# Kernel optimization log

Measured on AMD Instinct MI355X. Metric: run time of the kernel, lower is better.

## Reference

```python
import jax, jax.numpy as jnp
import numpy as np

TAU = 1.0
PAD_IDX = 0
EOS_IDX = 3
NEG = -10000000.0

B, T, H, E, V, BN = 256, 256, 1024, 512, 32000, 512


def setup_inputs() -> dict:
    key = jax.random.key(0)
    ks = jax.random.split(key, 30)
    s = lambda *sh: 0.02
    inp = {}
    inp['input_ids'] = jax.random.randint(ks[0], (B,), 0, V)
    inp['prediction'] = jax.random.normal(ks[1], (B, V), jnp.float32)
    inp['context'] = jax.random.normal(ks[2], (B, T, 2 * H), jnp.float32)
    inp['h0'] = jax.random.normal(ks[3], (2, B, H), jnp.float32)
    inp['mask'] = jax.random.randint(ks[4], (B, 8), 0, V)
    # parameters
    inp['embedding'] = jax.random.normal(ks[5], (V, E), jnp.float32) * 0.02
    inp['ge1_w'] = jax.random.normal(ks[6], (E, E), jnp.float32) * 0.02
    inp['ge1_b'] = jnp.zeros((E,), jnp.float32)
    inp['ge2_w'] = jax.random.normal(ks[7], (E, E), jnp.float32) * 0.02
    inp['ge2_b'] = jnp.zeros((E,), jnp.float32)
    inp['att_we'] = jax.random.normal(ks[8], (2 * H, H), jnp.float32) * 0.02
    inp['att_wd'] = jax.random.normal(ks[9], (H, H), jnp.float32) * 0.02
    inp['att_v'] = jax.random.normal(ks[10], (H,), jnp.float32) * 0.02
    in0 = 2 * H + E
    inp['wih0'] = jax.random.normal(ks[11], (3 * H, in0), jnp.float32) * 0.02
    inp['whh0'] = jax.random.normal(ks[12], (3 * H, H), jnp.float32) * 0.02
    inp['bih0'] = jnp.zeros((3 * H,), jnp.float32)
    inp['bhh0'] = jnp.zeros((3 * H,), jnp.float32)
    inp['wih1'] = jax.random.normal(ks[13], (3 * H, H), jnp.float32) * 0.02
    inp['whh1'] = jax.random.normal(ks[14], (3 * H, H), jnp.float32) * 0.02
    inp['bih1'] = jnp.zeros((3 * H,), jnp.float32)
    inp['bhh1'] = jnp.zeros((3 * H,), jnp.float32)
    inp['bn0_w'] = jax.random.normal(ks[15], (3 * H + E, BN), jnp.float32) * 0.02
    inp['bn0_b'] = jnp.zeros((BN,), jnp.float32)
    inp['bn1_w'] = jax.random.normal(ks[16], (BN, V), jnp.float32) * 0.02
    inp['bn1_b'] = jnp.zeros((V,), jnp.float32)
    return inp


def _gru_cell(x, h, wih, whh, bih, bhh):
    gi = x @ wih.T + bih  # [B, 3H]
    gh = h @ whh.T + bhh
    gi_r, gi_z, gi_n = jnp.split(gi, 3, axis=1)
    gh_r, gh_z, gh_n = jnp.split(gh, 3, axis=1)
    r = jax.nn.sigmoid(gi_r + gh_r)
    z = jax.nn.sigmoid(gi_z + gh_z)
    n = jnp.tanh(gi_n + r * gh_n)
    return (1.0 - z) * n + z * h


def _forward(input_ids, prediction, context, h0, mask, embedding,
             ge1_w, ge1_b, ge2_w, ge2_b, att_we, att_wd, att_v,
             wih0, whh0, bih0, bhh0, wih1, whh1, bih1, bhh1,
             bn0_w, bn0_b, bn1_w, bn1_b):
    embs = embedding[input_ids]  # [B, E]
    # global embedding gate
    probs = jax.nn.softmax(prediction / TAU, axis=1)  # [B, V]
    emb_avg = probs @ embedding  # [B, E]
    Hg = jax.nn.sigmoid(embs @ ge1_w + ge1_b + emb_avg @ ge2_w + ge2_b)
    embs = Hg * embs + (1.0 - Hg) * emb_avg
    # bahdanau attention with query = top-layer hidden
    q = h0[-1]  # [B, H]
    scores = jnp.tanh(context @ att_we + (q @ att_wd)[:, None, :]) @ att_v  # [B, T]
    attn = jax.nn.softmax(scores, axis=1)
    c_t = jnp.einsum('bt,btd->bd', attn, context)  # [B, 2H]
    rnn_in = jnp.concatenate([embs, c_t], axis=1)  # [B, E+2H]
    h1_0 = _gru_cell(rnn_in, h0[0], wih0, whh0, bih0, bhh0)
    h1_1 = _gru_cell(h1_0, h0[1], wih1, whh1, bih1, bhh1)
    output = h1_1
    h1 = jnp.stack([h1_0, h1_1])
    b0 = jnp.tanh(jnp.concatenate([output, c_t, embs], axis=1) @ bn0_w + bn0_b)
    pred = b0 @ bn1_w + bn1_b  # [B, V]
    # masked scatter: forbid already-generated tokens, but keep PAD/EOS columns
    pad_col = pred[:, PAD_IDX]
    eos_col = pred[:, EOS_IDX]
    rows = jnp.arange(pred.shape[0])
    pred = pred.at[rows[:, None], mask].set(NEG)
    pred = pred.at[:, PAD_IDX].set(pad_col)
    pred = pred.at[:, EOS_IDX].set(eos_col)
    return pred, h1, attn


def reference(input_ids, prediction, context, h0, mask, embedding,
              ge1_w, ge1_b, ge2_w, ge2_b, att_we, att_wd, att_v,
              wih0, whh0, bih0, bhh0, wih1, whh1, bih1, bhh1,
              bn0_w, bn0_b, bn1_w, bn1_b):
    return _forward(input_ids, prediction, context, h0, mask, embedding,
                    ge1_w, ge1_b, ge2_w, ge2_b, att_we, att_wd, att_v,
                    wih0, whh0, bih0, bhh0, wih1, whh1, bih1, bhh1,
                    bn0_w, bn0_b, bn1_w, bn1_b)
```

## Files before the change

### kernel.cpp

```cpp
#include <hip/hip_runtime.h>
#include <hip/hip_bf16.h>


typedef unsigned short u16;
typedef unsigned int u32;
typedef float f32x4 __attribute__((ext_vector_type(4)));
typedef u32 u32x4 __attribute__((ext_vector_type(4)));
typedef __bf16 bf16x8 __attribute__((ext_vector_type(8)));
typedef short s16x8 __attribute__((ext_vector_type(8)));

__device__ __forceinline__ u16 f2bf(float x) {
  u32 u = __float_as_uint(x);
  u += 0x7fffu + ((u >> 16) & 1u);
  return (u16)(u >> 16);
}
__device__ __forceinline__ u32 pack2(float a, float b) {
  return (u32)f2bf(a) | ((u32)f2bf(b) << 16);
}
__device__ __forceinline__ u32 cvt2(float a, float b) {
  union { __bf16 h[2]; u32 w; } u;
  u.h[0] = (__bf16)a; u.h[1] = (__bf16)b;
  return u.w;
}
__device__ __forceinline__ float bf2f(u16 v) {
  return __uint_as_float((u32)v << 16);
}
__device__ __forceinline__ f32x4 mfma_bf16(s16x8 a, s16x8 b, f32x4 c) {
  union { s16x8 s; bf16x8 b; } ua, ub;
  ua.s = a; ub.s = b;
  return __builtin_amdgcn_mfma_f32_16x16x32_bf16(ua.b, ub.b, c, 0, 0, 0);
}
__device__ __forceinline__ void gll16(const void* g, void* l) {
  __builtin_amdgcn_global_load_lds((__attribute__((address_space(1))) void*)g,
                                   (__attribute__((address_space(3))) void*)l,
                                   16, 0, 0);
}
__device__ __forceinline__ float sigf(float x) { return 1.0f / (1.0f + __expf(-x)); }

__global__ __launch_bounds__(256) void k_cvt8(const float* __restrict__ s,
                                              u16* __restrict__ d)
{
  size_t i = ((size_t)blockIdx.x * 256 + threadIdx.x) * 8;
  const size_t stride = (size_t)gridDim.x * 2048;
  for (; i < 134217728ull; i += stride) {
    float4 a = *(const float4*)(s + i);
    float4 b = *(const float4*)(s + i + 4);
    u32x4 w = {cvt2(a.x, a.y), cvt2(a.z, a.w), cvt2(b.x, b.y), cvt2(b.z, b.w)};
    *(u32x4*)(d + i) = w;
  }
}

__global__ __launch_bounds__(512, 4) void k_scores_bf(
    const u16* __restrict__ A, const u16* __restrict__ weT,
    const float* __restrict__ qd, const float* __restrict__ att_v,
    float* __restrict__ scores)
{
  __shared__ u16 As[2][4096];
  __shared__ u16 Bs[2][8192];

  const int tid = threadIdx.x;
  const int lane = tid & 63, wid = tid >> 6;
  const int l15 = lane & 15, lg = lane >> 4;
  const int wm = wid >> 2, wn = wid & 3;
  const int n0 = blockIdx.x * 256;
  const int m0 = blockIdx.y * 128;
  const int b = blockIdx.y >> 1;

  const int sslot = ((lane & 3) ^ ((lane >> 3) & 3)) * 8;
  const size_t asrc = (size_t)(m0 + wid * 16 + (lane >> 2)) * 2048 + sslot;
  size_t bsrc[2];
#pragma unroll
  for (int i = 0; i < 2; ++i)
    bsrc[i] = (size_t)(n0 + (wid * 2 + i) * 16 + (lane >> 2)) * 2048 + sslot;

  const int rslot = (lg ^ ((l15 >> 1) & 3)) * 8;
  int aoff[4], boff[4];
#pragma unroll
  for (int mf = 0; mf < 4; ++mf) aoff[mf] = (wm * 64 + mf * 16 + l15) * 32 + rslot;
#pragma unroll
  for (int nf = 0; nf < 4; ++nf) boff[nf] = (wn * 64 + nf * 16 + l15) * 32 + rslot;

  f32x4 acc[4][4];
#pragma unroll
  for (int mf = 0; mf < 4; ++mf)
#pragma unroll
    for (int nf = 0; nf < 4; ++nf) acc[mf][nf] = (f32x4){0.f, 0.f, 0.f, 0.f};

  {
    gll16(A + asrc, &As[0][wid * 512]);
#pragma unroll
    for (int i = 0; i < 2; ++i)
      gll16(weT + bsrc[i], &Bs[0][(wid * 2 + i) * 512]);
  }
  __syncthreads();

  for (int kt = 0; kt < 64; ++kt) {
    const int cur = kt & 1, nxt = cur ^ 1;
    if (kt < 63) {
      gll16(A + asrc + (size_t)(kt + 1) * 32, &As[nxt][wid * 512]);
#pragma unroll
      for (int i = 0; i < 2; ++i)
        gll16(weT + bsrc[i] + (size_t)(kt + 1) * 32, &Bs[nxt][(wid * 2 + i) * 512]);
    }
    s16x8 af[4], bf[4];
#pragma unroll
    for (int mf = 0; mf < 4; ++mf) af[mf] = *(const s16x8*)(&As[cur][0] + aoff[mf]);
#pragma unroll
    for (int nf = 0; nf < 4; ++nf) bf[nf] = *(const s16x8*)(&Bs[cur][0] + boff[nf]);
    __builtin_amdgcn_s_setprio(1);
#pragma unroll
    for (int nf = 0; nf < 4; ++nf)
#pragma unroll
      for (int mf = 0; mf < 4; ++mf)
        acc[mf][nf] = mfma_bf16(af[mf], bf[nf], acc[mf][nf]);
    __builtin_amdgcn_s_setprio(0);
    __syncthreads();
  }

  float rp[4][4] = {{0.f, 0.f, 0.f, 0.f}, {0.f, 0.f, 0.f, 0.f},
                    {0.f, 0.f, 0.f, 0.f}, {0.f, 0.f, 0.f, 0.f}};
#pragma unroll
  for (int nf = 0; nf < 4; ++nf) {
    int col = n0 + wn * 64 + nf * 16 + l15;
    float qv = qd[(size_t)b * 1024 + col];
    float vv = att_v[col];
#pragma unroll
    for (int mf = 0; mf < 4; ++mf)
#pragma unroll
      for (int e = 0; e < 4; ++e)
        rp[mf][e] += tanhf(acc[mf][nf][e] + qv) * vv;
  }
#pragma unroll
  for (int d = 1; d < 16; d <<= 1)
#pragma unroll
    for (int mf = 0; mf < 4; ++mf)
#pragma unroll
      for (int e = 0; e < 4; ++e)
        rp[mf][e] += __shfl_xor(rp[mf][e], d);
  if (l15 == 0) {
#pragma unroll
    for (int mf = 0; mf < 4; ++mf)
#pragma unroll
      for (int e = 0; e < 4; ++e)
        atomicAdd(&scores[(size_t)m0 + wm * 64 + mf * 16 + lg * 4 + e], rp[mf][e]);
  }
}

__global__ __launch_bounds__(256, 3) void k_scores(
    const float* __restrict__ ctx, const u16* __restrict__ weT,
    const float* __restrict__ qd, const float* __restrict__ att_v,
    float* __restrict__ scores)
{
  __shared__ u16 As[2][4096];
  __shared__ u16 Bs[2][4096];

  const int tid = threadIdx.x;
  const int lane = tid & 63, wid = tid >> 6;
  const int l15 = lane & 15, lg = lane >> 4;
  const int wm = wid >> 1, wn = wid & 1;
  const int n0 = blockIdx.x * 128;
  const int m0 = blockIdx.y * 128;
  const int b = blockIdx.y >> 1;

  const int r0 = tid >> 3, c4 = tid & 7;
  const float* actx = ctx + (size_t)(m0 + r0) * 2048 + c4 * 4;
  const int awoff = r0 * 32 + c4 * 4;

  size_t bsrc[2];
#pragma unroll
  for (int i = 0; i < 2; ++i)
    bsrc[i] = (size_t)(n0 + (wid * 2 + i) * 16 + (lane >> 2)) * 2048 + (size_t)(lane & 3) * 8;

  int aoff[4], boff[4];
#pragma unroll
  for (int mf = 0; mf < 4; ++mf) aoff[mf] = (wm * 64 + mf * 16 + l15) * 32 + lg * 8;
#pragma unroll
  for (int nf = 0; nf < 4; ++nf) boff[nf] = (wn * 64 + nf * 16 + l15) * 32 + lg * 8;

  f32x4 acc[4][4];
#pragma unroll
  for (int mf = 0; mf < 4; ++mf)
#pragma unroll
    for (int nf = 0; nf < 4; ++nf) acc[mf][nf] = (f32x4){0.f, 0.f, 0.f, 0.f};

  {
#pragma unroll
    for (int i = 0; i < 2; ++i)
      gll16(weT + bsrc[i], &Bs[0][(wid * 2 + i) * 512]);
#pragma unroll
    for (int j = 0; j < 4; ++j) {
      float4 av = *(const float4*)(actx + (size_t)(j * 32) * 2048);
      u32* w = (u32*)&As[0][awoff + j * 1024];
      w[0] = cvt2(av.x, av.y); w[1] = cvt2(av.z, av.w);
    }
  }
  __syncthreads();

  for (int kt = 0; kt < 64; ++kt) {
    const int cur = kt & 1, nxt = cur ^ 1;
    const bool pf = (kt < 63);
    float4 av[4];
    if (pf) {
#pragma unroll
      for (int i = 0; i < 2; ++i)
        gll16(weT + bsrc[i] + (size_t)(kt + 1) * 32, &Bs[nxt][(wid * 2 + i) * 512]);
#pragma unroll
      for (int j = 0; j < 4; ++j)
        av[j] = *(const float4*)(actx + (size_t)(j * 32) * 2048 + (kt + 1) * 32);
    }
    s16x8 af[4], bf[4];
#pragma unroll
    for (int mf = 0; mf < 4; ++mf) af[mf] = *(const s16x8*)(&As[cur][0] + aoff[mf]);
#pragma unroll
    for (int nf = 0; nf < 4; ++nf) bf[nf] = *(const s16x8*)(&Bs[cur][0] + boff[nf]);
#pragma unroll
    for (int nf = 0; nf < 4; ++nf)
#pragma unroll
      for (int mf = 0; mf < 4; ++mf)
        acc[mf][nf] = mfma_bf16(af[mf], bf[nf], acc[mf][nf]);
    if (pf) {
#pragma unroll
      for (int j = 0; j < 4; ++j) {
        u32* w = (u32*)&As[nxt][awoff + j * 1024];
        w[0] = cvt2(av[j].x, av[j].y); w[1] = cvt2(av[j].z, av[j].w);
      }
    }
    __syncthreads();
  }

  float rp[4][4] = {{0.f, 0.f, 0.f, 0.f}, {0.f, 0.f, 0.f, 0.f},
                    {0.f, 0.f, 0.f, 0.f}, {0.f, 0.f, 0.f, 0.f}};
#pragma unroll
  for (int nf = 0; nf < 4; ++nf) {
    int col = n0 + wn * 64 + nf * 16 + l15;
    float qv = qd[(size_t)b * 1024 + col];
    float vv = att_v[col];
#pragma unroll
    for (int mf = 0; mf < 4; ++mf)
#pragma unroll
      for (int e = 0; e < 4; ++e)
        rp[mf][e] += tanhf(acc[mf][nf][e] + qv) * vv;
  }
#pragma unroll
  for (int d = 1; d < 16; d <<= 1)
#pragma unroll
    for (int mf = 0; mf < 4; ++mf)
#pragma unroll
      for (int e = 0; e < 4; ++e)
        rp[mf][e] += __shfl_xor(rp[mf][e], d);
  if (l15 == 0) {
#pragma unroll
    for (int mf = 0; mf < 4; ++mf)
#pragma unroll
      for (int e = 0; e < 4; ++e)
        atomicAdd(&scores[(size_t)m0 + wm * 64 + mf * 16 + lg * 4 + e], rp[mf][e]);
  }
}

template <int MODE>
__global__ __launch_bounds__(256, 2) void k_gemm(
    const u16* __restrict__ A, const float* __restrict__ W,
    float* __restrict__ C, const float* __restrict__ bias,
    int N, int K, int ksteps_per, int tot_ksteps, int atomic_mode)
{
  __shared__ u16 As[2][8192];
  __shared__ u16 Bs[2][2048];
  const int tid = threadIdx.x, lane = tid & 63, wid = tid >> 6;
  const int l15 = lane & 15, lg = lane >> 4;
  const int m0 = blockIdx.x * 256;
  const int n0 = blockIdx.y * 64;
  const int kc0 = blockIdx.z * ksteps_per;
  int kcn = tot_ksteps - kc0;
  if (kcn > ksteps_per) kcn = ksteps_per;

  size_t asrc[4];
#pragma unroll
  for (int j = 0; j < 4; ++j)
    asrc[j] = (size_t)(m0 + wid * 64 + j * 16 + (lane >> 2)) * K + (size_t)(lane & 3) * 8;
  int aoff[4], boff[4];
#pragma unroll
  for (int mf = 0; mf < 4; ++mf) aoff[mf] = (wid * 64 + mf * 16 + l15) * 32 + lg * 8;
#pragma unroll
  for (int nf = 0; nf < 4; ++nf) boff[nf] = (nf * 16 + l15) * 32 + lg * 8;

  const int b_row = tid >> 2, b_c8 = tid & 3;
  const int b_kk = tid >> 3, b_c4 = tid & 7;

  f32x4 acc[4][4];
#pragma unroll
  for (int mf = 0; mf < 4; ++mf)
#pragma unroll
    for (int nf = 0; nf < 4; ++nf) acc[mf][nf] = (f32x4){0.f, 0.f, 0.f, 0.f};

  {
#pragma unroll
    for (int j = 0; j < 4; ++j)
      gll16(A + asrc[j] + (size_t)kc0 * 32, &As[0][wid * 2048 + j * 512]);
    if (MODE == 0) {
      const float* p = W + (size_t)(n0 + b_row) * K + (size_t)kc0 * 32 + b_c8 * 8;
      float4 v0 = *(const float4*)p, v1 = *(const float4*)(p + 4);
      u32* w = (u32*)&Bs[0][b_row * 32 + b_c8 * 8];
      w[0] = pack2(v0.x, v0.y); w[1] = pack2(v0.z, v0.w);
      w[2] = pack2(v1.x, v1.y); w[3] = pack2(v1.z, v1.w);
    } else {
      const float* p = W + (size_t)(kc0 * 32 + b_kk) * N + n0 + b_c4 * 4;
      float4 v0 = *(const float4*)p;
      float4 v1 = *(const float4*)(p + 32);
      int r0 = b_c4 * 4, r1 = 32 + b_c4 * 4;
      Bs[0][(r0 + 0) * 32 + b_kk] = f2bf(v0.x);
      Bs[0][(r0 + 1) * 32 + b_kk] = f2bf(v0.y);
      Bs[0][(r0 + 2) * 32 + b_kk] = f2bf(v0.z);
      Bs[0][(r0 + 3) * 32 + b_kk] = f2bf(v0.w);
      Bs[0][(r1 + 0) * 32 + b_kk] = f2bf(v1.x);
      Bs[0][(r1 + 1) * 32 + b_kk] = f2bf(v1.y);
      Bs[0][(r1 + 2) * 32 + b_kk] = f2bf(v1.z);
      Bs[0][(r1 + 3) * 32 + b_kk] = f2bf(v1.w);
    }
  }
  __syncthreads();

  for (int s = 0; s < kcn; ++s) {
    const int cur = s & 1, nxt = cur ^ 1;
    const bool pf = (s + 1 < kcn);
    const int ktn = kc0 + s + 1;
    float4 v0, v1;
    if (pf) {
#pragma unroll
      for (int j = 0; j < 4; ++j)
        gll16(A + asrc[j] + (size_t)ktn * 32, &As[nxt][wid * 2048 + j * 512]);
      if (MODE == 0) {
        const float* p = W + (size_t)(n0 + b_row) * K + (size_t)ktn * 32 + b_c8 * 8;
        v0 = *(const float4*)p; v1 = *(const float4*)(p + 4);
      } else {
        const float* p = W + (size_t)(ktn * 32 + b_kk) * N + n0 + b_c4 * 4;
        v0 = *(const float4*)p;
        v1 = *(const float4*)(p + 32);
      }
    }
    s16x8 af[4], bf[4];
#pragma unroll
    for (int mf = 0; mf < 4; ++mf) af[mf] = *(const s16x8*)(&As[cur][0] + aoff[mf]);
#pragma unroll
    for (int nf = 0; nf < 4; ++nf) bf[nf] = *(const s16x8*)(&Bs[cur][0] + boff[nf]);
#pragma unroll
    for (int nf = 0; nf < 4; ++nf)
#pragma unroll
      for (int mf = 0; mf < 4; ++mf)
        acc[mf][nf] = mfma_bf16(af[mf], bf[nf], acc[mf][nf]);
    if (pf) {
      if (MODE == 0) {
        u32* w = (u32*)&Bs[nxt][b_row * 32 + b_c8 * 8];
        w[0] = pack2(v0.x, v0.y); w[1] = pack2(v0.z, v0.w);
        w[2] = pack2(v1.x, v1.y); w[3] = pack2(v1.z, v1.w);
      } else {
        int r0 = b_c4 * 4, r1 = 32 + b_c4 * 4;
        Bs[nxt][(r0 + 0) * 32 + b_kk] = f2bf(v0.x);
        Bs[nxt][(r0 + 1) * 32 + b_kk] = f2bf(v0.y);
        Bs[nxt][(r0 + 2) * 32 + b_kk] = f2bf(v0.z);
        Bs[nxt][(r0 + 3) * 32 + b_kk] = f2bf(v0.w);
        Bs[nxt][(r1 + 0) * 32 + b_kk] = f2bf(v1.x);
        Bs[nxt][(r1 + 1) * 32 + b_kk] = f2bf(v1.y);
        Bs[nxt][(r1 + 2) * 32 + b_kk] = f2bf(v1.z);
        Bs[nxt][(r1 + 3) * 32 + b_kk] = f2bf(v1.w);
      }
    }
    __syncthreads();
  }

  const size_t Ns = (size_t)N;
#pragma unroll
  for (int mf = 0; mf < 4; ++mf)
#pragma unroll
    for (int nf = 0; nf < 4; ++nf) {
      int col = n0 + nf * 16 + l15;
#pragma unroll
      for (int e = 0; e < 4; ++e) {
        int row = m0 + wid * 64 + mf * 16 + lg * 4 + e;
        float v = acc[mf][nf][e];
        if (atomic_mode) atomicAdd(&C[row * Ns + col], v);
        else C[row * Ns + col] = v + (bias ? bias[col] : 0.0f);
      }
    }
}

__global__ __launch_bounds__(256) void k_twe(const float* __restrict__ we, u16* __restrict__ weT)
{
  __shared__ float t[32][33];
  const int n0 = blockIdx.x * 32, k0 = blockIdx.y * 32;
  const int tid = threadIdx.x;
#pragma unroll
  for (int p = 0; p < 4; ++p) {
    int e = tid + p * 256, r = e >> 5, c = e & 31;
    t[r][c] = we[(size_t)(k0 + r) * 1024 + n0 + c];
  }
  __syncthreads();
#pragma unroll
  for (int p = 0; p < 4; ++p) {
    int e = tid + p * 256, n = e >> 5, k = e & 31;
    weT[(size_t)(n0 + n) * 2048 + k0 + k] = f2bf(t[k][n]);
  }
}

__global__ void k_cast(const float* __restrict__ s, u16* __restrict__ d, int n)
{
  int i = blockIdx.x * 256 + threadIdx.x;
  if (i < n) d[i] = f2bf(s[i]);
}

__global__ void k_gather(const int* __restrict__ ids, const float* __restrict__ emb,
                         float* __restrict__ e0, u16* __restrict__ e0b)
{
  int b = blockIdx.x, tid = threadIdx.x;
  int id = ids[b];
  for (int i = tid; i < 512; i += 256) {
    float v = emb[(size_t)id * 512 + i];
    e0[(size_t)b * 512 + i] = v;
    e0b[(size_t)b * 512 + i] = f2bf(v);
  }
}

__global__ __launch_bounds__(256) void k_softmax_pred(const float* __restrict__ pred,
                                                      u16* __restrict__ probs)
{
  __shared__ float sm[4];
  const int row = blockIdx.x, tid = threadIdx.x;
  const float* x = pred + (size_t)row * 32000;
  float mx = -1e30f;
  for (int i = tid; i < 32000; i += 256) mx = fmaxf(mx, x[i]);
#pragma unroll
  for (int d = 1; d < 64; d <<= 1) mx = fmaxf(mx, __shfl_xor(mx, d));
  if ((tid & 63) == 0) sm[tid >> 6] = mx;
  __syncthreads();
  mx = fmaxf(fmaxf(sm[0], sm[1]), fmaxf(sm[2], sm[3]));
  float s = 0.f;
  for (int i = tid; i < 32000; i += 256) s += __expf(x[i] - mx);
#pragma unroll
  for (int d = 1; d < 64; d <<= 1) s += __shfl_xor(s, d);
  __syncthreads();
  if ((tid & 63) == 0) sm[tid >> 6] = s;
  __syncthreads();
  s = sm[0] + sm[1] + sm[2] + sm[3];
  float inv = 1.0f / s;
  for (int i = tid; i < 32000; i += 256)
    probs[(size_t)row * 32000 + i] = f2bf(__expf(x[i] - mx) * inv);
}

__global__ __launch_bounds__(256) void k_softmax_sc(const float* __restrict__ sc,
                                                    float* __restrict__ attn)
{
  __shared__ float sm[4];
  const int row = blockIdx.x, tid = threadIdx.x;
  float x = sc[(size_t)row * 256 + tid];
  float mx = x;
#pragma unroll
  for (int d = 1; d < 64; d <<= 1) mx = fmaxf(mx, __shfl_xor(mx, d));
  if ((tid & 63) == 0) sm[tid >> 6] = mx;
  __syncthreads();
  mx = fmaxf(fmaxf(sm[0], sm[1]), fmaxf(sm[2], sm[3]));
  float e = __expf(x - mx);
  float s = e;
#pragma unroll
  for (int d = 1; d < 64; d <<= 1) s += __shfl_xor(s, d);
  __syncthreads();
  if ((tid & 63) == 0) sm[tid >> 6] = s;
  __syncthreads();
  s = sm[0] + sm[1] + sm[2] + sm[3];
  attn[(size_t)row * 256 + tid] = e / s;
}

__global__ __launch_bounds__(256) void k_ct_bf(const u16* __restrict__ ctxb,
                                               const float* __restrict__ attn,
                                               float* __restrict__ c_t)
{
  const int b = blockIdx.y;
  const int d0 = blockIdx.x * 512 + threadIdx.x * 2;
  const u16* cp = ctxb + (size_t)b * 524288 + d0;
  const float* ar = attn + (size_t)b * 256;
  float a0 = 0.f, a1 = 0.f;
#pragma unroll 8
  for (int t = 0; t < 256; ++t) {
    float a = ar[t];
    ushort2 v = *(const ushort2*)(cp + (size_t)t * 2048);
    a0 += a * bf2f(v.x); a1 += a * bf2f(v.y);
  }
  float2* o = (float2*)(c_t + (size_t)b * 2048 + d0);
  *o = (float2){a0, a1};
}

__global__ __launch_bounds__(256) void k_ct(const float* __restrict__ ctx,
                                            const float* __restrict__ attn,
                                            float* __restrict__ c_t)
{
  const int b = blockIdx.y;
  const int d0 = blockIdx.x * 512 + threadIdx.x * 2;
  const float2* cp = (const float2*)(ctx + (size_t)b * 524288 + d0);
  const float* ar = attn + (size_t)b * 256;
  float ax = 0.f, ay = 0.f;
#pragma unroll 4
  for (int t = 0; t < 256; ++t) {
    float a = ar[t];
    float2 v = cp[(size_t)t * 1024];
    ax += a * v.x; ay += a * v.y;
  }
  c_t[(size_t)b * 2048 + d0] = ax;
  c_t[(size_t)b * 2048 + d0 + 1] = ay;
}

__global__ void k_gate(const float* __restrict__ gepre, const float* __restrict__ b1,
                       const float* __restrict__ b2, const float* __restrict__ e0,
                       const float* __restrict__ ea, float* __restrict__ embs)
{
  int i = blockIdx.x * 256 + threadIdx.x;
  int nn = i & 511;
  float hg = sigf(gepre[i] + b1[nn] + b2[nn]);
  embs[i] = hg * e0[i] + (1.0f - hg) * ea[i];
}

__global__ void k_cat_rnn(const float* __restrict__ embs, const float* __restrict__ ct,
                          u16* __restrict__ out)
{
  int i = blockIdx.x * 256 + threadIdx.x;
  int m = i / 2560, c = i - m * 2560;
  float v = (c < 512) ? embs[(size_t)m * 512 + c] : ct[(size_t)m * 2048 + (c - 512)];
  out[i] = f2bf(v);
}

__global__ void k_gru(const float* __restrict__ gi, const float* __restrict__ gh,
                      const float* __restrict__ bih, const float* __restrict__ bhh,
                      const float* __restrict__ hprev, float* __restrict__ hout,
                      u16* __restrict__ hout_bf)
{
  int i = blockIdx.x * 256 + threadIdx.x;
  int m = i >> 10, h = i & 1023;
  const float* gim = gi + (size_t)m * 3072;
  const float* ghm = gh + (size_t)m * 3072;
  float r = sigf(gim[h] + bih[h] + ghm[h] + bhh[h]);
  float z = sigf(gim[1024 + h] + bih[1024 + h] + ghm[1024 + h] + bhh[1024 + h]);
  float n = tanhf(gim[2048 + h] + bih[2048 + h] + r * (ghm[2048 + h] + bhh[2048 + h]));
  float hv = (1.0f - z) * n + z * hprev[i];
  hout[i] = hv;
  if (hout_bf) hout_bf[i] = f2bf(hv);
}

__global__ void k_cat_bn0(const float* __restrict__ h11, const float* __restrict__ ct,
                          const float* __restrict__ embs, u16* __restrict__ out)
{
  int i = blockIdx.x * 256 + threadIdx.x;
  int m = i / 3584, c = i - m * 3584;
  float v;
  if (c < 1024) v = h11[(size_t)m * 1024 + c];
  else if (c < 3072) v = ct[(size_t)m * 2048 + (c - 1024)];
  else v = embs[(size_t)m * 512 + (c - 3072)];
  out[i] = f2bf(v);
}

__global__ void k_bn0(const float* __restrict__ pre, const float* __restrict__ bias,
                      u16* __restrict__ b0b)
{
  int i = blockIdx.x * 256 + threadIdx.x;
  int nn = i & 511;
  b0b[i] = f2bf(tanhf(pre[i] + bias[nn]));
}

__global__ void k_mask(const int* __restrict__ mask, float* __restrict__ pred)
{
  int t = blockIdx.x * 256 + threadIdx.x;
  if (t >= 2048) return;
  int b = t >> 3;
  int col = mask[t];
  if (col != 0 && col != 3) pred[(size_t)b * 32000 + col] = -10000000.0f;
}

extern "C" void kernel_launch(void* const* d_in, const int* in_sizes, int n_in,
                              void* d_out, int out_size, void* d_ws, size_t ws_size,
                              hipStream_t stream)
{
  const int*   input_ids = (const int*)d_in[0];
  const float* prediction= (const float*)d_in[1];
  const float* context   = (const float*)d_in[2];
  const float* h0        = (const float*)d_in[3];
  const int*   maskp     = (const int*)d_in[4];
  const float* embedding = (const float*)d_in[5];
  const float* ge1_w = (const float*)d_in[6];
  const float* ge1_b = (const float*)d_in[7];
  const float* ge2_w = (const float*)d_in[8];
  const float* ge2_b = (const float*)d_in[9];
  const float* att_we = (const float*)d_in[10];
  const float* att_wd = (const float*)d_in[11];
  const float* att_v  = (const float*)d_in[12];
  const float* wih0 = (const float*)d_in[13];
  const float* whh0 = (const float*)d_in[14];
  const float* bih0 = (const float*)d_in[15];
  const float* bhh0 = (const float*)d_in[16];
  const float* wih1 = (const float*)d_in[17];
  const float* whh1 = (const float*)d_in[18];
  const float* bih1 = (const float*)d_in[19];
  const float* bhh1 = (const float*)d_in[20];
  const float* bn0_w = (const float*)d_in[21];
  const float* bn0_b = (const float*)d_in[22];
  const float* bn1_w = (const float*)d_in[23];
  const float* bn1_b = (const float*)d_in[24];

  float* out = (float*)d_out;
  float* out_pred = out;
  float* out_h1_0 = out + 8192000;
  float* out_h1_1 = out + 8454144;
  float* out_attn = out + 8716288;

  char* ws = (char*)d_ws;
  float* qd      = (float*)(ws + 0);
  float* emb_avg = (float*)(ws + 1048576);
  float* gepre   = (float*)(ws + 1572864);
  float* gi0     = (float*)(ws + 2097152);
  float* gh0     = (float*)(ws + 5242880);
  float* gi1     = (float*)(ws + 8388608);
  float* gh1     = (float*)(ws + 11534336);
  float* bn0pre  = (float*)(ws + 14680064);
  float* scores  = (float*)(ws + 15204352);
  const size_t MS_BYTES = 15466496;
  float* c_t     = (float*)(ws + 15466496);
  float* embs0   = (float*)(ws + 17563648);
  float* embs    = (float*)(ws + 18087936);
  u16* weT       = (u16*)(ws + 18612224);
  u16* h0_bf     = (u16*)(ws + 22806528);
  u16* embs0_bf  = (u16*)(ws + 23855104);
  u16* probs_bf  = (u16*)(ws + 24117248);
  u16* embavg_bf = (u16*)(ws + 40501248);
  u16* rnnin_bf  = (u16*)(ws + 40763392);
  u16* h1_0_bf   = (u16*)(ws + 42074112);
  u16* bn0in_bf  = (u16*)(ws + 42598400);
  u16* b0_bf     = (u16*)(ws + 44433408);
  u16* ctx_bf    = (u16*)(ws + 44695552);
  const bool big = ws_size >= 44695552ull + 268435456ull;

  (void)in_sizes; (void)n_in; (void)out_size;

  hipMemsetAsync(ws, 0, MS_BYTES, stream);

  if (big) k_cvt8<<<8192, 256, 0, stream>>>(context, ctx_bf);
  k_twe<<<dim3(32, 64), 256, 0, stream>>>(att_we, weT);
  k_cast<<<2048, 256, 0, stream>>>(h0, h0_bf, 524288);
  k_gather<<<256, 256, 0, stream>>>(input_ids, embedding, embs0, embs0_bf);
  k_softmax_pred<<<256, 256, 0, stream>>>(prediction, probs_bf);

  k_gemm<1><<<dim3(1, 16, 8), 256, 0, stream>>>(h0_bf + 262144, att_wd, qd, nullptr,
                                                1024, 1024, 4, 32, 1);
  if (big)
    k_scores_bf<<<dim3(4, 512), 512, 0, stream>>>(ctx_bf, weT, qd, att_v, scores);
  else
    k_scores<<<dim3(8, 512), 256, 0, stream>>>(context, weT, qd, att_v, scores);

  k_gemm<1><<<dim3(1, 8, 50), 256, 0, stream>>>(probs_bf, embedding, emb_avg, nullptr,
                                                512, 32000, 20, 1000, 1);
  k_cast<<<512, 256, 0, stream>>>(emb_avg, embavg_bf, 131072);
  k_gemm<1><<<dim3(1, 8, 4), 256, 0, stream>>>(embs0_bf, ge1_w, gepre, nullptr,
                                               512, 512, 4, 16, 1);
  k_gemm<1><<<dim3(1, 8, 4), 256, 0, stream>>>(embavg_bf, ge2_w, gepre, nullptr,
                                               512, 512, 4, 16, 1);
  k_gate<<<512, 256, 0, stream>>>(gepre, ge1_b, ge2_b, embs0, emb_avg, embs);

  k_softmax_sc<<<256, 256, 0, stream>>>(scores, out_attn);
  if (big)
    k_ct_bf<<<dim3(4, 256), 256, 0, stream>>>(ctx_bf, out_attn, c_t);
  else
    k_ct<<<dim3(4, 256), 256, 0, stream>>>(context, out_attn, c_t);

  k_cat_rnn<<<2560, 256, 0, stream>>>(embs, c_t, rnnin_bf);
  k_gemm<0><<<dim3(1, 48, 5), 256, 0, stream>>>(rnnin_bf, wih0, gi0, nullptr,
                                                3072, 2560, 16, 80, 1);
  k_gemm<0><<<dim3(1, 48, 4), 256, 0, stream>>>(h0_bf, whh0, gh0, nullptr,
                                                3072, 1024, 8, 32, 1);
  k_gru<<<1024, 256, 0, stream>>>(gi0, gh0, bih0, bhh0, h0, out_h1_0, h1_0_bf);
  k_gemm<0><<<dim3(1, 48, 4), 256, 0, stream>>>(h1_0_bf, wih1, gi1, nullptr,
                                                3072, 1024, 8, 32, 1);
  k_gemm<0><<<dim3(1, 48, 4), 256, 0, stream>>>(h0_bf + 262144, whh1, gh1, nullptr,
                                                3072, 1024, 8, 32, 1);
  k_gru<<<1024, 256, 0, stream>>>(gi1, gh1, bih1, bhh1, h0 + 262144, out_h1_1, nullptr);

  k_cat_bn0<<<3584, 256, 0, stream>>>(out_h1_1, c_t, embs, bn0in_bf);
  k_gemm<1><<<dim3(1, 8, 16), 256, 0, stream>>>(bn0in_bf, bn0_w, bn0pre, nullptr,
                                                512, 3584, 7, 112, 1);
  k_bn0<<<512, 256, 0, stream>>>(bn0pre, bn0_b, b0_bf);
  k_gemm<1><<<dim3(1, 500, 1), 256, 0, stream>>>(b0_bf, bn1_w, out_pred, bn1_b,
                                                 32000, 512, 16, 16, 0);
  k_mask<<<8, 256, 0, stream>>>(maskp, out_pred);
}
```

Before: 885.2 us.

## Triple-buffer scores GEMM, remap tiles per XCD, fuse small prep and softmax kernels

The attention-scores GEMM moves from double to triple buffering, waiting on vmcnt instead of a full syncthreads, and its 1D grid is remapped so M tiles are spread across XCDs. The weight transpose, h0 cast and embedding gather are merged into one prep kernel. Attention softmax is fused into the context-vector kernel, and the gate is fused with the RNN-input concat. The prediction softmax now uses 1024 threads, an online max/sum in one pass and an LDS-cached bf16 copy of the row. Together these aim to cut launch count, global re-reads and per-step sync stalls, at the cost of more LDS use and softmax inputs rounded to bf16 before exp.

```diff
diff --git a/kernel.cpp b/kernel.cpp
--- a/kernel.cpp
+++ b/kernel.cpp
@@ -55,16 +55,21 @@
     const float* __restrict__ qd, const float* __restrict__ att_v,
     float* __restrict__ scores)
 {
-  __shared__ u16 As[2][4096];
-  __shared__ u16 Bs[2][8192];
+  __shared__ u16 As[3][4096];
+  __shared__ u16 Bs[3][8192];
 
   const int tid = threadIdx.x;
   const int lane = tid & 63, wid = tid >> 6;
   const int l15 = lane & 15, lg = lane >> 4;
   const int wm = wid >> 2, wn = wid & 3;
-  const int n0 = blockIdx.x * 256;
-  const int m0 = blockIdx.y * 128;
-  const int b = blockIdx.y >> 1;
+
+  const int f = blockIdx.x;
+  const int xcd = f & 7, slot = f >> 3;
+  const int ntile = slot & 3;
+  const int mtile = (slot >> 2) * 8 + xcd;
+  const int n0 = ntile * 256;
+  const int m0 = mtile * 128;
+  const int b = mtile >> 1;
 
   const int sslot = ((lane & 3) ^ ((lane >> 3) & 3)) * 8;
   const size_t asrc = (size_t)(m0 + wid * 16 + (lane >> 2)) * 2048 + sslot;
@@ -86,27 +91,40 @@
 #pragma unroll
     for (int nf = 0; nf < 4; ++nf) acc[mf][nf] = (f32x4){0.f, 0.f, 0.f, 0.f};
 
+  u16* As0 = &As[0][0];
+  u16* Bs0 = &Bs[0][0];
+
   {
-    gll16(A + asrc, &As[0][wid * 512]);
+    gll16(A + asrc, As0 + wid * 512);
 #pragma unroll
     for (int i = 0; i < 2; ++i)
-      gll16(weT + bsrc[i], &Bs[0][(wid * 2 + i) * 512]);
-  }
-  __syncthreads();
-
+      gll16(weT + bsrc[i], Bs0 + (wid * 2 + i) * 512);
+    gll16(A + asrc + 32, As0 + 4096 + wid * 512);
+#pragma unroll
+    for (int i = 0; i < 2; ++i)
+      gll16(weT + bsrc[i] + 32, Bs0 + 8192 + (wid * 2 + i) * 512);
+  }
+
+  int cur = 0, stg = 2;
   for (int kt = 0; kt < 64; ++kt) {
-    const int cur = kt & 1, nxt = cur ^ 1;
-    if (kt < 63) {
-      gll16(A + asrc + (size_t)(kt + 1) * 32, &As[nxt][wid * 512]);
+    if (kt < 63) asm volatile("s_waitcnt vmcnt(3)" ::: "memory");
+    else         asm volatile("s_waitcnt vmcnt(0)" ::: "memory");
+    __builtin_amdgcn_s_barrier();
+    __builtin_amdgcn_sched_barrier(0);
+    if (kt + 2 < 64) {
+      gll16(A + asrc + (size_t)(kt + 2) * 32, As0 + stg * 4096 + wid * 512);
 #pragma unroll
       for (int i = 0; i < 2; ++i)
-        gll16(weT + bsrc[i] + (size_t)(kt + 1) * 32, &Bs[nxt][(wid * 2 + i) * 512]);
+        gll16(weT + bsrc[i] + (size_t)(kt + 2) * 32,
+              Bs0 + stg * 8192 + (wid * 2 + i) * 512);
     }
     s16x8 af[4], bf[4];
 #pragma unroll
-    for (int mf = 0; mf < 4; ++mf) af[mf] = *(const s16x8*)(&As[cur][0] + aoff[mf]);
-#pragma unroll
-    for (int nf = 0; nf < 4; ++nf) bf[nf] = *(const s16x8*)(&Bs[cur][0] + boff[nf]);
+    for (int mf = 0; mf < 4; ++mf)
+      af[mf] = *(const s16x8*)(As0 + cur * 4096 + aoff[mf]);
+#pragma unroll
+    for (int nf = 0; nf < 4; ++nf)
+      bf[nf] = *(const s16x8*)(Bs0 + cur * 8192 + boff[nf]);
     __builtin_amdgcn_s_setprio(1);
 #pragma unroll
     for (int nf = 0; nf < 4; ++nf)
@@ -114,7 +132,8 @@
       for (int mf = 0; mf < 4; ++mf)
         acc[mf][nf] = mfma_bf16(af[mf], bf[nf], acc[mf][nf]);
     __builtin_amdgcn_s_setprio(0);
-    __syncthreads();
+    cur = (cur == 2) ? 0 : cur + 1;
+    stg = (stg == 2) ? 0 : stg + 1;
   }
 
   float rp[4][4] = {{0.f, 0.f, 0.f, 0.f}, {0.f, 0.f, 0.f, 0.f},
@@ -383,21 +402,38 @@
     }
 }
 
-__global__ __launch_bounds__(256) void k_twe(const float* __restrict__ we, u16* __restrict__ weT)
+__global__ __launch_bounds__(256) void k_prep(
+    const float* __restrict__ we, u16* __restrict__ weT,
+    const float* __restrict__ h0, u16* __restrict__ h0_bf,
+    const int* __restrict__ ids, const float* __restrict__ emb,
+    float* __restrict__ e0, u16* __restrict__ e0b)
 {
   __shared__ float t[32][33];
-  const int n0 = blockIdx.x * 32, k0 = blockIdx.y * 32;
-  const int tid = threadIdx.x;
-#pragma unroll
-  for (int p = 0; p < 4; ++p) {
-    int e = tid + p * 256, r = e >> 5, c = e & 31;
-    t[r][c] = we[(size_t)(k0 + r) * 1024 + n0 + c];
-  }
-  __syncthreads();
-#pragma unroll
-  for (int p = 0; p < 4; ++p) {
-    int e = tid + p * 256, n = e >> 5, k = e & 31;
-    weT[(size_t)(n0 + n) * 2048 + k0 + k] = f2bf(t[k][n]);
+  const int bid = blockIdx.x, tid = threadIdx.x;
+  if (bid < 2048) {
+    const int n0 = (bid & 31) * 32, k0 = (bid >> 5) * 32;
+#pragma unroll
+    for (int p = 0; p < 4; ++p) {
+      int e = tid + p * 256, r = e >> 5, c = e & 31;
+      t[r][c] = we[(size_t)(k0 + r) * 1024 + n0 + c];
+    }
+    __syncthreads();
+#pragma unroll
+    for (int p = 0; p < 4; ++p) {
+      int e = tid + p * 256, n = e >> 5, k = e & 31;
+      weT[(size_t)(n0 + n) * 2048 + k0 + k] = f2bf(t[k][n]);
+    }
+  } else if (bid < 4096) {
+    int i = (bid - 2048) * 256 + tid;
+    h0_bf[i] = f2bf(h0[i]);
+  } else {
+    int b = bid - 4096;
+    int id = ids[b];
+    for (int i = tid; i < 512; i += 256) {
+      float v = emb[(size_t)id * 512 + i];
+      e0[(size_t)b * 512 + i] = v;
+      e0b[(size_t)b * 512 + i] = f2bf(v);
+    }
   }
 }
 
@@ -407,42 +443,39 @@
   if (i < n) d[i] = f2bf(s[i]);
 }
 
-__global__ void k_gather(const int* __restrict__ ids, const float* __restrict__ emb,
-                         float* __restrict__ e0, u16* __restrict__ e0b)
-{
-  int b = blockIdx.x, tid = threadIdx.x;
-  int id = ids[b];
-  for (int i = tid; i < 512; i += 256) {
-    float v = emb[(size_t)id * 512 + i];
-    e0[(size_t)b * 512 + i] = v;
-    e0b[(size_t)b * 512 + i] = f2bf(v);
-  }
-}
-
-__global__ __launch_bounds__(256) void k_softmax_pred(const float* __restrict__ pred,
-                                                      u16* __restrict__ probs)
-{
-  __shared__ float sm[4];
+__global__ __launch_bounds__(1024) void k_softmax_pred(const float* __restrict__ pred,
+                                                       u16* __restrict__ probs)
+{
+  __shared__ u16 xrow[32000];
+  __shared__ float smM[16], smS[16];
   const int row = blockIdx.x, tid = threadIdx.x;
   const float* x = pred + (size_t)row * 32000;
-  float mx = -1e30f;
-  for (int i = tid; i < 32000; i += 256) mx = fmaxf(mx, x[i]);
-#pragma unroll
-  for (int d = 1; d < 64; d <<= 1) mx = fmaxf(mx, __shfl_xor(mx, d));
-  if ((tid & 63) == 0) sm[tid >> 6] = mx;
-  __syncthreads();
-  mx = fmaxf(fmaxf(sm[0], sm[1]), fmaxf(sm[2], sm[3]));
-  float s = 0.f;
-  for (int i = tid; i < 32000; i += 256) s += __expf(x[i] - mx);
-#pragma unroll
-  for (int d = 1; d < 64; d <<= 1) s += __shfl_xor(s, d);
-  __syncthreads();
-  if ((tid & 63) == 0) sm[tid >> 6] = s;
-  __syncthreads();
-  s = sm[0] + sm[1] + sm[2] + sm[3];
-  float inv = 1.0f / s;
-  for (int i = tid; i < 32000; i += 256)
-    probs[(size_t)row * 32000 + i] = f2bf(__expf(x[i] - mx) * inv);
+  float m = -3.0e38f, s = 0.f;
+  for (int i = tid; i < 32000; i += 1024) {
+    u16 bv = f2bf(x[i]);
+    xrow[i] = bv;
+    float vr = bf2f(bv);
+    if (vr > m) { s = s * __expf(m - vr) + 1.0f; m = vr; }
+    else s += __expf(vr - m);
+  }
+#pragma unroll
+  for (int d = 1; d < 64; d <<= 1) {
+    float mo = __shfl_xor(m, d), so = __shfl_xor(s, d);
+    float M = fmaxf(m, mo);
+    s = s * __expf(m - M) + so * __expf(mo - M);
+    m = M;
+  }
+  if ((tid & 63) == 0) { smM[tid >> 6] = m; smS[tid >> 6] = s; }
+  __syncthreads();
+  float M = -3.0e38f;
+#pragma unroll
+  for (int w = 0; w < 16; ++w) M = fmaxf(M, smM[w]);
+  float S = 0.f;
+#pragma unroll
+  for (int w = 0; w < 16; ++w) S += smS[w] * __expf(smM[w] - M);
+  float inv = 1.0f / S;
+  for (int i = tid; i < 32000; i += 1024)
+    probs[(size_t)row * 32000 + i] = f2bf(__expf(bf2f(xrow[i]) - M) * inv);
 }
 
 __global__ __launch_bounds__(256) void k_softmax_sc(const float* __restrict__ sc,
@@ -468,20 +501,41 @@
   attn[(size_t)row * 256 + tid] = e / s;
 }
 
-__global__ __launch_bounds__(256) void k_ct_bf(const u16* __restrict__ ctxb,
-                                               const float* __restrict__ attn,
-                                               float* __restrict__ c_t)
-{
-  const int b = blockIdx.y;
-  const int d0 = blockIdx.x * 512 + threadIdx.x * 2;
+__global__ __launch_bounds__(256) void k_attn_ct(
+    const float* __restrict__ sc, const u16* __restrict__ ctxb,
+    float* __restrict__ attn, float* __restrict__ c_t)
+{
+  __shared__ float sm[4];
+  __shared__ float att[256];
+  const int b = blockIdx.y, tid = threadIdx.x;
+  float x = sc[(size_t)b * 256 + tid];
+  float mx = x;
+#pragma unroll
+  for (int d = 1; d < 64; d <<= 1) mx = fmaxf(mx, __shfl_xor(mx, d));
+  if ((tid & 63) == 0) sm[tid >> 6] = mx;
+  __syncthreads();
+  mx = fmaxf(fmaxf(sm[0], sm[1]), fmaxf(sm[2], sm[3]));
+  float e = __expf(x - mx);
+  float s = e;
+#pragma unroll
+  for (int d = 1; d < 64; d <<= 1) s += __shfl_xor(s, d);
+  __syncthreads();
+  if ((tid & 63) == 0) sm[tid >> 6] = s;
+  __syncthreads();
+  s = sm[0] + sm[1] + sm[2] + sm[3];
+  float a = e / s;
+  att[tid] = a;
+  if (blockIdx.x == 0) attn[(size_t)b * 256 + tid] = a;
+  __syncthreads();
+
+  const int d0 = blockIdx.x * 512 + tid * 2;
   const u16* cp = ctxb + (size_t)b * 524288 + d0;
-  const float* ar = attn + (size_t)b * 256;
   float a0 = 0.f, a1 = 0.f;
 #pragma unroll 8
   for (int t = 0; t < 256; ++t) {
-    float a = ar[t];
+    float av = att[t];
     ushort2 v = *(const ushort2*)(cp + (size_t)t * 2048);
-    a0 += a * bf2f(v.x); a1 += a * bf2f(v.y);
+    a0 += av * bf2f(v.x); a1 += av * bf2f(v.y);
   }
   float2* o = (float2*)(c_t + (size_t)b * 2048 + d0);
   *o = (float2){a0, a1};
@@ -506,22 +560,22 @@
   c_t[(size_t)b * 2048 + d0 + 1] = ay;
 }
 
-__global__ void k_gate(const float* __restrict__ gepre, const float* __restrict__ b1,
-                       const float* __restrict__ b2, const float* __restrict__ e0,
-                       const float* __restrict__ ea, float* __restrict__ embs)
-{
-  int i = blockIdx.x * 256 + threadIdx.x;
-  int nn = i & 511;
-  float hg = sigf(gepre[i] + b1[nn] + b2[nn]);
-  embs[i] = hg * e0[i] + (1.0f - hg) * ea[i];
-}
-
-__global__ void k_cat_rnn(const float* __restrict__ embs, const float* __restrict__ ct,
-                          u16* __restrict__ out)
+__global__ void k_gate_cat(const float* __restrict__ gepre, const float* __restrict__ b1,
+                           const float* __restrict__ b2, const float* __restrict__ e0,
+                           const float* __restrict__ ea, float* __restrict__ embs,
+                           const float* __restrict__ ct, u16* __restrict__ out)
 {
   int i = blockIdx.x * 256 + threadIdx.x;
   int m = i / 2560, c = i - m * 2560;
-  float v = (c < 512) ? embs[(size_t)m * 512 + c] : ct[(size_t)m * 2048 + (c - 512)];
+  float v;
+  if (c < 512) {
+    int idx = m * 512 + c;
+    float hg = sigf(gepre[idx] + b1[c] + b2[c]);
+    v = hg * e0[idx] + (1.0f - hg) * ea[idx];
+    embs[idx] = v;
+  } else {
+    v = ct[(size_t)m * 2048 + (c - 512)];
+  }
   out[i] = f2bf(v);
 }
 
@@ -638,15 +692,14 @@
   hipMemsetAsync(ws, 0, MS_BYTES, stream);
 
   if (big) k_cvt8<<<8192, 256, 0, stream>>>(context, ctx_bf);
-  k_twe<<<dim3(32, 64), 256, 0, stream>>>(att_we, weT);
-  k_cast<<<2048, 256, 0, stream>>>(h0, h0_bf, 524288);
-  k_gather<<<256, 256, 0, stream>>>(input_ids, embedding, embs0, embs0_bf);
-  k_softmax_pred<<<256, 256, 0, stream>>>(prediction, probs_bf);
+  k_prep<<<4352, 256, 0, stream>>>(att_we, weT, h0, h0_bf, input_ids, embedding,
+                                   embs0, embs0_bf);
+  k_softmax_pred<<<256, 1024, 0, stream>>>(prediction, probs_bf);
 
   k_gemm<1><<<dim3(1, 16, 8), 256, 0, stream>>>(h0_bf + 262144, att_wd, qd, nullptr,
                                                 1024, 1024, 4, 32, 1);
   if (big)
-    k_scores_bf<<<dim3(4, 512), 512, 0, stream>>>(ctx_bf, weT, qd, att_v, scores);
+    k_scores_bf<<<2048, 512, 0, stream>>>(ctx_bf, weT, qd, att_v, scores);
   else
     k_scores<<<dim3(8, 512), 256, 0, stream>>>(context, weT, qd, att_v, scores);
 
@@ -657,15 +710,17 @@
                                                512, 512, 4, 16, 1);
   k_gemm<1><<<dim3(1, 8, 4), 256, 0, stream>>>(embavg_bf, ge2_w, gepre, nullptr,
                                                512, 512, 4, 16, 1);
-  k_gate<<<512, 256, 0, stream>>>(gepre, ge1_b, ge2_b, embs0, emb_avg, embs);
-
-  k_softmax_sc<<<256, 256, 0, stream>>>(scores, out_attn);
-  if (big)
-    k_ct_bf<<<dim3(4, 256), 256, 0, stream>>>(ctx_bf, out_attn, c_t);
-  else
+
+  if (big) {
+    k_attn_ct<<<dim3(4, 256), 256, 0, stream>>>(scores, ctx_bf, out_attn, c_t);
+  } else {
+    k_softmax_sc<<<256, 256, 0, stream>>>(scores, out_attn);
     k_ct<<<dim3(4, 256), 256, 0, stream>>>(context, out_attn, c_t);
-
-  k_cat_rnn<<<2560, 256, 0, stream>>>(embs, c_t, rnnin_bf);
+  }
+
+  k_gate_cat<<<2560, 256, 0, stream>>>(gepre, ge1_b, ge2_b, embs0, emb_avg,
+                                       embs, c_t, rnnin_bf);
+
   k_gemm<0><<<dim3(1, 48, 5), 256, 0, stream>>>(rnnin_bf, wih0, gi0, nullptr,
                                                 3072, 2560, 16, 80, 1);
   k_gemm<0><<<dim3(1, 48, 4), 256, 0, stream>>>(h0_bf, whh0, gh0, nullptr,
```

After: 802.2 us. -9.4%, faster.
